# Kernel tuning notes

Measured on AMD Instinct MI355X. Metric: run time of the kernel, lower is better.

## Reference

```python
import jax, jax.numpy as jnp
import numpy as np

N_SAMPLES = 50
BETA = 1.0
EPSILON = 1e-6

def setup_inputs() -> dict:
    key = jax.random.key(0)
    k1, k2, k3, k4 = jax.random.split(key, 4)
    B, D = 8192, 64
    mean = jax.random.normal(k1, (B, D), dtype=jnp.float32)
    variance = jax.random.uniform(k2, (B, D), dtype=jnp.float32)
    noise = jax.random.normal(k3, (N_SAMPLES, B, D), dtype=jnp.float32)
    target = jax.random.normal(k4, (B, D), dtype=jnp.float32)
    return {"mean": mean, "variance": variance, "noise": noise, "target": target}

def reference(mean, variance, noise, target):
    n = noise.shape[0]
    std = jnp.sqrt(variance + EPSILON)                      # [B, D]
    samples = mean[None] + noise * std[None]                # [n, B, D]
    # E[||X - y||] (elementwise abs, mean over samples)
    first_term = jnp.abs(samples - target[None]).mean(axis=0)  # [B, D]
    # sum_{i<j} |s_i - s_j| via sort identity: for sorted x, equals sum_k (2k - n + 1) x_k
    s_sorted = jnp.sort(samples, axis=0)                    # [n, B, D]
    coef = (2.0 * jnp.arange(n, dtype=s_sorted.dtype) - (n - 1))  # [n]
    pair_sum = jnp.einsum('s,sbd->bd', coef, s_sorted)      # [B, D]
    n_pairs = n * (n - 1) / 2.0
    second_term = pair_sum / n_pairs
    energy_score = first_term - (BETA / 2.0) * second_term  # [B, D]
    return energy_score.mean()                               # reduction='mean'
```

## Files before the change

kernel.cpp:

```cpp
#include <hip/hip_runtime.h>
#include <float.h>

#define NS 50
#define NP 64
#define B_DIM 8192
#define D_DIM 64
#define BD (B_DIM * D_DIM)
#define BLOCK 256
#define EPT 2
#define GRIDN (BD / (BLOCK * EPT))

typedef __fp16 f16x2 __attribute__((ext_vector_type(2)));

__device__ __forceinline__ float block_reduce(float e, int tid) {
    #pragma unroll
    for (int off = 32; off > 0; off >>= 1)
        e += __shfl_down(e, off, 64);
    __shared__ float wsum[BLOCK / 64];
    const int lane = tid & 63;
    const int wid  = tid >> 6;
    if (lane == 0) wsum[wid] = e;
    __syncthreads();
    float bs = 0.0f;
    if (tid == 0) {
        #pragma unroll
        for (int w = 0; w < BLOCK / 64; ++w) bs += wsum[w];
    }
    return bs;
}

__device__ __forceinline__ float energy_pair_packed(
    const float* __restrict__ mean, const float* __restrict__ variance,
    const float* __restrict__ noise, const float* __restrict__ target,
    int col0) {

    const float2 mv = *(const float2*)(mean + col0);
    const float2 vv = *(const float2*)(variance + col0);
    const float2 tv = *(const float2*)(target + col0);
    float mA = mv.x, mB = mv.y;
    float tA = tv.x, tB = tv.y;
    float sdA = sqrtf(vv.x + 1e-6f);
    float sdB = sqrtf(vv.y + 1e-6f);
    asm volatile("" : "+v"(mA), "+v"(tA), "+v"(sdA), "+v"(mB), "+v"(tB), "+v"(sdB));

    float2 f2[NS];
    const unsigned voff = (unsigned)col0 * 4u;
    #pragma unroll
    for (int k = 0; k < NS; ++k) {
        const unsigned ok = voff + (unsigned)k * (unsigned)(BD * 4);
        asm volatile("global_load_dwordx2 %0, %1, %2"
                     : "=v"(f2[k]) : "v"(ok), "s"(noise));
    }
    asm volatile("s_waitcnt vmcnt(0)" ::: "memory");
    __builtin_amdgcn_sched_barrier(0);

    float fA0 = 0.0f, fA1 = 0.0f, fB0 = 0.0f, fB1 = 0.0f;
    f16x2 p[NP];
    #pragma unroll
    for (int k = 0; k < NS; ++k) {
        float sa = fmaf(f2[k].x, sdA, mA);
        float sb = fmaf(f2[k].y, sdB, mB);
        float dA = fabsf(sa - tA);
        float dB = fabsf(sb - tB);
        if (k & 1) { fA1 += dA; fB1 += dB; }
        else       { fA0 += dA; fB0 += dB; }
        p[k] = __builtin_amdgcn_cvt_pkrtz(sa, sb);
    }
    const f16x2 pad = {(__fp16)65504.0f, (__fp16)65504.0f};
    #pragma unroll
    for (int k = NS; k < NP; ++k) p[k] = pad;

    #pragma unroll
    for (int k = 2; k <= NP; k <<= 1) {
        #pragma unroll
        for (int j = k >> 1; j > 0; j >>= 1) {
            #pragma unroll
            for (int i = 0; i < NP; ++i) {
                const int l = i ^ j;
                if (l > i) {
                    const bool up = ((i & k) == 0);
                    f16x2 x = p[i], y = p[l];
                    f16x2 lo = __builtin_elementwise_min(x, y);
                    f16x2 hi = __builtin_elementwise_max(x, y);
                    p[i] = up ? lo : hi;
                    p[l] = up ? hi : lo;
                }
            }
        }
    }

    float pA0 = 0.0f, pA1 = 0.0f, pB0 = 0.0f, pB1 = 0.0f;
    #pragma unroll
    for (int k = 0; k < NS; ++k) {
        const float c = (float)(2 * k - (NS - 1));
        float sa = (float)p[k][0];
        float sb = (float)p[k][1];
        if (k & 1) { pA1 = fmaf(c, sa, pA1); pB1 = fmaf(c, sb, pB1); }
        else       { pA0 = fmaf(c, sa, pA0); pB0 = fmaf(c, sb, pB0); }
    }

    float e = (fA0 + fA1 + fB0 + fB1) * (1.0f / NS)
            - (pA0 + pA1 + pB0 + pB1) * (1.0f / 2450.0f);
    return e * (1.0f / (float)BD);
}

__global__ __launch_bounds__(BLOCK, 2) void energy_partial_kernel(
    const float* __restrict__ mean, const float* __restrict__ variance,
    const float* __restrict__ noise, const float* __restrict__ target,
    float* __restrict__ partial) {
    const int tid  = threadIdx.x;
    const int wg   = (blockIdx.x & 7) * (GRIDN / 8) + (blockIdx.x >> 3);
    const int col0 = wg * (BLOCK * EPT) + tid * EPT;
    float e = energy_pair_packed(mean, variance, noise, target, col0);
    float bs = block_reduce(e, tid);
    if (tid == 0) partial[blockIdx.x] = bs;
}

__global__ __launch_bounds__(BLOCK) void reduce_partial_kernel(
    const float* __restrict__ partial, float* __restrict__ out) {
    float e = 0.0f;
    #pragma unroll
    for (int i = 0; i < GRIDN / BLOCK; ++i)
        e += partial[i * BLOCK + threadIdx.x];
    float bs = block_reduce(e, threadIdx.x);
    if (threadIdx.x == 0) out[0] = bs;
}

__global__ __launch_bounds__(BLOCK, 2) void energy_atomic_kernel(
    const float* __restrict__ mean, const float* __restrict__ variance,
    const float* __restrict__ noise, const float* __restrict__ target,
    float* __restrict__ out) {
    const int tid  = threadIdx.x;
    const int wg   = (blockIdx.x & 7) * (GRIDN / 8) + (blockIdx.x >> 3);
    const int col0 = wg * (BLOCK * EPT) + tid * EPT;
    float e = energy_pair_packed(mean, variance, noise, target, col0);
    float bs = block_reduce(e, tid);
    if (tid == 0) atomicAdd(out, bs);
}

extern "C" void kernel_launch(void* const* d_in, const int* in_sizes, int n_in,
                              void* d_out, int out_size, void* d_ws, size_t ws_size,
                              hipStream_t stream) {
    const float* mean     = (const float*)d_in[0];
    const float* variance = (const float*)d_in[1];
    const float* noise    = (const float*)d_in[2];
    const float* target   = (const float*)d_in[3];
    float* out = (float*)d_out;

    if (ws_size >= (size_t)GRIDN * sizeof(float)) {
        float* partial = (float*)d_ws;
        energy_partial_kernel<<<GRIDN, BLOCK, 0, stream>>>(mean, variance, noise,
                                                           target, partial);
        reduce_partial_kernel<<<1, BLOCK, 0, stream>>>(partial, out);
    } else {
        (void)hipMemsetAsync(out, 0, sizeof(float), stream);
        energy_atomic_kernel<<<GRIDN, BLOCK, 0, stream>>>(mean, variance, noise,
                                                          target, out);
    }
}
```

Baseline: 28.45 us.

## Process two column pairs per thread, overlapping second noise load with first sort

Each thread now handles four columns as two pairs. The noise loads for the second pair are issued before the first pair is sorted and summed, so memory latency can hide behind the sorting-network arithmetic. The grid is halved to 512 workgroups, and the coefficient and abs sums are merged across lanes before accumulation. In exchange, register pressure rises because two 50-element buffers are live at once, there are fewer waves to hide latency, and the work per thread is longer.

Measured after the change: 31.17 us. 9.6% more time.

```diff
diff --git a/kernel.cpp b/kernel.cpp
--- a/kernel.cpp
+++ b/kernel.cpp
@@ -7,8 +7,7 @@
 #define D_DIM 64
 #define BD (B_DIM * D_DIM)
 #define BLOCK 256
-#define EPT 2
-#define GRIDN (BD / (BLOCK * EPT))
+#define GRIDW 512
 
 typedef __fp16 f16x2 __attribute__((ext_vector_type(2)));
 
@@ -29,47 +28,28 @@
     return bs;
 }
 
-__device__ __forceinline__ float energy_pair_packed(
-    const float* __restrict__ mean, const float* __restrict__ variance,
-    const float* __restrict__ noise, const float* __restrict__ target,
-    int col0) {
-
-    const float2 mv = *(const float2*)(mean + col0);
-    const float2 vv = *(const float2*)(variance + col0);
-    const float2 tv = *(const float2*)(target + col0);
-    float mA = mv.x, mB = mv.y;
-    float tA = tv.x, tB = tv.y;
-    float sdA = sqrtf(vv.x + 1e-6f);
-    float sdB = sqrtf(vv.y + 1e-6f);
-    asm volatile("" : "+v"(mA), "+v"(tA), "+v"(sdA), "+v"(mB), "+v"(tB), "+v"(sdB));
-
-    float2 f2[NS];
-    const unsigned voff = (unsigned)col0 * 4u;
-    #pragma unroll
-    for (int k = 0; k < NS; ++k) {
-        const unsigned ok = voff + (unsigned)k * (unsigned)(BD * 4);
-        asm volatile("global_load_dwordx2 %0, %1, %2"
-                     : "=v"(f2[k]) : "v"(ok), "s"(noise));
-    }
-    asm volatile("s_waitcnt vmcnt(0)" ::: "memory");
-    __builtin_amdgcn_sched_barrier(0);
-
-    float fA0 = 0.0f, fA1 = 0.0f, fB0 = 0.0f, fB1 = 0.0f;
-    f16x2 p[NP];
+__device__ __forceinline__ void pack_pair(const float2* f2, f16x2* p,
+                                          float mA, float sdA, float tA,
+                                          float mB, float sdB, float tB,
+                                          float& first) {
+    float f0 = 0.0f, f1 = 0.0f;
     #pragma unroll
     for (int k = 0; k < NS; ++k) {
         float sa = fmaf(f2[k].x, sdA, mA);
         float sb = fmaf(f2[k].y, sdB, mB);
         float dA = fabsf(sa - tA);
         float dB = fabsf(sb - tB);
-        if (k & 1) { fA1 += dA; fB1 += dB; }
-        else       { fA0 += dA; fB0 += dB; }
+        if (k & 1) f1 += dA + dB;
+        else       f0 += dA + dB;
         p[k] = __builtin_amdgcn_cvt_pkrtz(sa, sb);
     }
     const f16x2 pad = {(__fp16)65504.0f, (__fp16)65504.0f};
     #pragma unroll
     for (int k = NS; k < NP; ++k) p[k] = pad;
-
+    first += f0 + f1;
+}
+
+__device__ __forceinline__ void sort_packed(f16x2* p) {
     #pragma unroll
     for (int k = 2; k <= NP; k <<= 1) {
         #pragma unroll
@@ -88,19 +68,78 @@
             }
         }
     }
-
-    float pA0 = 0.0f, pA1 = 0.0f, pB0 = 0.0f, pB1 = 0.0f;
+}
+
+__device__ __forceinline__ float coef_sum(const f16x2* p) {
+    float p0 = 0.0f, p1 = 0.0f;
     #pragma unroll
     for (int k = 0; k < NS; ++k) {
         const float c = (float)(2 * k - (NS - 1));
-        float sa = (float)p[k][0];
-        float sb = (float)p[k][1];
-        if (k & 1) { pA1 = fmaf(c, sa, pA1); pB1 = fmaf(c, sb, pB1); }
-        else       { pA0 = fmaf(c, sa, pA0); pB0 = fmaf(c, sb, pB0); }
-    }
-
-    float e = (fA0 + fA1 + fB0 + fB1) * (1.0f / NS)
-            - (pA0 + pA1 + pB0 + pB1) * (1.0f / 2450.0f);
+        float s = (float)p[k][0] + (float)p[k][1];
+        if (k & 1) p1 = fmaf(c, s, p1);
+        else       p0 = fmaf(c, s, p0);
+    }
+    return p0 + p1;
+}
+
+__device__ __forceinline__ float energy_quad(
+    const float* __restrict__ mean, const float* __restrict__ variance,
+    const float* __restrict__ noise, const float* __restrict__ target,
+    int colA, int colB) {
+
+    const float2 mvA = *(const float2*)(mean + colA);
+    const float2 vvA = *(const float2*)(variance + colA);
+    const float2 tvA = *(const float2*)(target + colA);
+    const float2 mvB = *(const float2*)(mean + colB);
+    const float2 vvB = *(const float2*)(variance + colB);
+    const float2 tvB = *(const float2*)(target + colB);
+    float mA0 = mvA.x, mA1 = mvA.y, tA0 = tvA.x, tA1 = tvA.y;
+    float mB0 = mvB.x, mB1 = mvB.y, tB0 = tvB.x, tB1 = tvB.y;
+    float sdA0 = sqrtf(vvA.x + 1e-6f), sdA1 = sqrtf(vvA.y + 1e-6f);
+    float sdB0 = sqrtf(vvB.x + 1e-6f), sdB1 = sqrtf(vvB.y + 1e-6f);
+    asm volatile("" : "+v"(mA0), "+v"(mA1), "+v"(tA0), "+v"(tA1),
+                      "+v"(sdA0), "+v"(sdA1));
+    asm volatile("" : "+v"(mB0), "+v"(mB1), "+v"(tB0), "+v"(tB1),
+                      "+v"(sdB0), "+v"(sdB1));
+
+    float first = 0.0f;
+
+    float2 fa[NS];
+    const unsigned offA = (unsigned)colA * 4u;
+    #pragma unroll
+    for (int k = 0; k < NS; ++k) {
+        const unsigned ok = offA + (unsigned)k * (unsigned)(BD * 4);
+        asm volatile("global_load_dwordx2 %0, %1, %2"
+                     : "=v"(fa[k]) : "v"(ok), "s"(noise));
+    }
+    asm volatile("s_waitcnt vmcnt(0)" ::: "memory");
+    __builtin_amdgcn_sched_barrier(0);
+    f16x2 pA[NP];
+    pack_pair(fa, pA, mA0, sdA0, tA0, mA1, sdA1, tA1, first);
+    __builtin_amdgcn_sched_barrier(0);
+
+    float2 fb[NS];
+    const unsigned offB = (unsigned)colB * 4u;
+    #pragma unroll
+    for (int k = 0; k < NS; ++k) {
+        const unsigned ok = offB + (unsigned)k * (unsigned)(BD * 4);
+        asm volatile("global_load_dwordx2 %0, %1, %2"
+                     : "=v"(fb[k]) : "v"(ok), "s"(noise));
+    }
+    __builtin_amdgcn_sched_barrier(0);
+
+    sort_packed(pA);
+    float pair = coef_sum(pA);
+    __builtin_amdgcn_sched_barrier(0);
+
+    asm volatile("s_waitcnt vmcnt(0)" ::: "memory");
+    __builtin_amdgcn_sched_barrier(0);
+    f16x2 pB[NP];
+    pack_pair(fb, pB, mB0, sdB0, tB0, mB1, sdB1, tB1, first);
+    sort_packed(pB);
+    pair += coef_sum(pB);
+
+    float e = first * (1.0f / NS) - pair * (1.0f / 2450.0f);
     return e * (1.0f / (float)BD);
 }
 
@@ -109,9 +148,11 @@
     const float* __restrict__ noise, const float* __restrict__ target,
     float* __restrict__ partial) {
     const int tid  = threadIdx.x;
-    const int wg   = (blockIdx.x & 7) * (GRIDN / 8) + (blockIdx.x >> 3);
-    const int col0 = wg * (BLOCK * EPT) + tid * EPT;
-    float e = energy_pair_packed(mean, variance, noise, target, col0);
+    const int wg   = (blockIdx.x & 7) * (GRIDW / 8) + (blockIdx.x >> 3);
+    const int base = wg * (BLOCK * 4);
+    const int colA = base + tid * 2;
+    const int colB = base + BLOCK * 2 + tid * 2;
+    float e = energy_quad(mean, variance, noise, target, colA, colB);
     float bs = block_reduce(e, tid);
     if (tid == 0) partial[blockIdx.x] = bs;
 }
@@ -120,7 +161,7 @@
     const float* __restrict__ partial, float* __restrict__ out) {
     float e = 0.0f;
     #pragma unroll
-    for (int i = 0; i < GRIDN / BLOCK; ++i)
+    for (int i = 0; i < GRIDW / BLOCK; ++i)
         e += partial[i * BLOCK + threadIdx.x];
     float bs = block_reduce(e, threadIdx.x);
     if (threadIdx.x == 0) out[0] = bs;
@@ -131,9 +172,11 @@
     const float* __restrict__ noise, const float* __restrict__ target,
     float* __restrict__ out) {
     const int tid  = threadIdx.x;
-    const int wg   = (blockIdx.x & 7) * (GRIDN / 8) + (blockIdx.x >> 3);
-    const int col0 = wg * (BLOCK * EPT) + tid * EPT;
-    float e = energy_pair_packed(mean, variance, noise, target, col0);
+    const int wg   = (blockIdx.x & 7) * (GRIDW / 8) + (blockIdx.x >> 3);
+    const int base = wg * (BLOCK * 4);
+    const int colA = base + tid * 2;
+    const int colB = base + BLOCK * 2 + tid * 2;
+    float e = energy_quad(mean, variance, noise, target, colA, colB);
     float bs = block_reduce(e, tid);
     if (tid == 0) atomicAdd(out, bs);
 }
@@ -147,14 +190,14 @@
     const float* target   = (const float*)d_in[3];
     float* out = (float*)d_out;
 
-    if (ws_size >= (size_t)GRIDN * sizeof(float)) {
+    if (ws_size >= (size_t)GRIDW * sizeof(float)) {
         float* partial = (float*)d_ws;
-        energy_partial_kernel<<<GRIDN, BLOCK, 0, stream>>>(mean, variance, noise,
+        energy_partial_kernel<<<GRIDW, BLOCK, 0, stream>>>(mean, variance, noise,
                                                            target, partial);
         reduce_partial_kernel<<<1, BLOCK, 0, stream>>>(partial, out);
     } else {
         (void)hipMemsetAsync(out, 0, sizeof(float), stream);
-        energy_atomic_kernel<<<GRIDN, BLOCK, 0, stream>>>(mean, variance, noise,
+        energy_atomic_kernel<<<GRIDW, BLOCK, 0, stream>>>(mean, variance, noise,
                                                           target, out);
     }
 }
```
